# Kernel tuning notes

Hardware: AMD Instinct MI355X
Metric: run time of the kernel (lower is better)

The kernel has to match this reference:

```python
import jax, jax.numpy as jnp
import numpy as np

B, S, E, H, FF = 4, 1024, 1024, 16, 4096
D = E // H
EPS = 1e-5


def layer_norm(x, g, b):
    m = jnp.mean(x, axis=-1, keepdims=True)
    v = jnp.var(x, axis=-1, keepdims=True)
    return (x - m) / jnp.sqrt(v + EPS) * g + b


def setup_inputs() -> dict:
    key = jax.random.key(0)
    ks = jax.random.split(key, 12)
    x = jax.random.normal(ks[0], (B, S, E), dtype=jnp.float32)
    # binary attention mask [B,S,S]; force diagonal=1 so no row is fully masked
    mask = jax.random.randint(ks[1], (B, S, S), 0, 2).astype(jnp.float32)
    idx = jnp.arange(S)
    mask = mask.at[:, idx, idx].set(1.0)
    gnn_adj = jax.random.normal(ks[2], (B, S, S), dtype=jnp.float32) * 0.02
    sc = 0.02
    params = dict(
        Wq=jax.random.normal(ks[3], (E, E), dtype=jnp.float32) * sc, bq=jnp.zeros((E,), jnp.float32),
        Wk=jax.random.normal(ks[4], (E, E), dtype=jnp.float32) * sc, bk=jnp.zeros((E,), jnp.float32),
        Wv=jax.random.normal(ks[5], (E, E), dtype=jnp.float32) * sc, bv=jnp.zeros((E,), jnp.float32),
        Wo=jax.random.normal(ks[6], (E, E), dtype=jnp.float32) * sc, bo=jnp.zeros((E,), jnp.float32),
        g1=jnp.ones((E,), jnp.float32), b1=jnp.zeros((E,), jnp.float32),
        g2=jnp.ones((E,), jnp.float32), b2=jnp.zeros((E,), jnp.float32),
        W1=jax.random.normal(ks[7], (E, FF), dtype=jnp.float32) * sc, bf1=jnp.zeros((FF,), jnp.float32),
        W2=jax.random.normal(ks[8], (FF, E), dtype=jnp.float32) * sc, bf2=jnp.zeros((E,), jnp.float32),
    )
    return dict(x=x, mask=mask, gnn_adj=gnn_adj, **params)


def reference(x, mask, gnn_adj, Wq, bq, Wk, bk, Wv, bv, Wo, bo, g1, b1, g2, b2, W1, bf1, W2, bf2):
    # pre-norm (norm_first=True), dropout = identity (eval)
    nx = layer_norm(x, g1, b1)
    # QKV projections -> [B,H,S,D]
    def split_heads(t):
        return t.reshape(B, S, H, D).transpose(0, 2, 1, 3)
    q = split_heads(nx @ Wq + bq)
    k = split_heads(nx @ Wk + bk)
    v = split_heads(nx @ Wv + bv)
    scores = jnp.einsum('bhqd,bhkd->bhqk', q, k) / jnp.sqrt(jnp.float32(D))
    m = mask[:, None]  # [B,1,S,S]
    scores = jnp.where(m == 0, -jnp.inf, scores * m)
    attn = jax.nn.softmax(scores, axis=-1)
    # non-standard: additive bias AFTER softmax
    attn = attn + gnn_adj[:, None]
    xv = jnp.einsum('bhqk,bhkd->bhqd', attn, v)
    xv = xv.transpose(0, 2, 1, 3).reshape(B, S, E)
    x = x + (xv @ Wo + bo)
    h = layer_norm(x, g2, b2)
    ff = jax.nn.gelu(h @ W1 + bf1, approximate=False) @ W2 + bf2
    return x + ff
```

## Files before the change

kernel.cpp:

```cpp
#include <hip/hip_runtime.h>
#include <hip/hip_bf16.h>

typedef unsigned short u16;
typedef short bf16x8 __attribute__((ext_vector_type(8)));
typedef float f32x4 __attribute__((ext_vector_type(4)));

#define B_ 4
#define S_ 1024
#define E_ 1024
#define H_ 16
#define FF_ 4096
#define D_ 64
#define M_ 4096

__device__ __forceinline__ u16 f2bf(float f) {
  unsigned int u = __builtin_bit_cast(unsigned int, f);
  u += 0x7fffu + ((u >> 16) & 1u);
  return (u16)(u >> 16);
}
__device__ __forceinline__ float bf2f(u16 v) {
  unsigned int u = ((unsigned int)v) << 16;
  return __builtin_bit_cast(float, u);
}

__device__ __forceinline__ void gld_lds16(const void* g, void* l) {
  __builtin_amdgcn_global_load_lds((__attribute__((address_space(1))) void*)g,
                                   (__attribute__((address_space(3))) void*)l,
                                   16, 0, 0);
}

__global__ void __launch_bounds__(256) pre_kernel(
    const float* __restrict__ wq, const float* __restrict__ wk,
    const float* __restrict__ wv, const float* __restrict__ wo,
    const float* __restrict__ w1, const float* __restrict__ w2,
    u16* __restrict__ wt,
    const float* __restrict__ x, const float* __restrict__ g1,
    const float* __restrict__ b1, u16* __restrict__ nx,
    const float* __restrict__ mask, const float* __restrict__ gnn,
    u16* __restrict__ biasI, u16* __restrict__ gnnbf) {
  __shared__ __attribute__((aligned(16))) float smem_f[1088];
  int bid = blockIdx.x;
  int t = threadIdx.x;
  if (bid < 12288) {
    const float* src; u16* dst; int K, N; int local;
    if (bid < 4096) {
      int wsel = bid >> 10; local = bid & 1023; K = 1024; N = 1024;
      src = wsel == 0 ? wq : wsel == 1 ? wk : wsel == 2 ? wv : wo;
      dst = wt + (size_t)wsel * 1024 * 1024;
    } else if (bid < 8192) {
      local = bid - 4096; K = 1024; N = 4096; src = w1;
      dst = wt + (size_t)4 * 1024 * 1024;
    } else {
      local = bid - 8192; K = 4096; N = 1024; src = w2;
      dst = wt + (size_t)8 * 1024 * 1024;
    }
    int tiles_n = N >> 5;
    int n0 = (local % tiles_n) << 5, k0 = (local / tiles_n) << 5;
    float (*tl)[33] = reinterpret_cast<float(*)[33]>(smem_f);
    int tx = t & 31, ty = t >> 5;
#pragma unroll
    for (int i = 0; i < 4; ++i)
      tl[ty + i * 8][tx] = src[(size_t)(k0 + ty + i * 8) * N + n0 + tx];
    __syncthreads();
#pragma unroll
    for (int i = 0; i < 4; ++i)
      dst[(size_t)(n0 + ty + i * 8) * K + k0 + tx] = f2bf(tl[tx][ty + i * 8]);
  } else if (bid < 16384) {
    int row = bid - 12288;
    const float* xr = x + (size_t)row * 1024;
    float4 v = *(const float4*)(xr + t * 4);
    float s = v.x + v.y + v.z + v.w;
    float q = v.x * v.x + v.y * v.y + v.z * v.z + v.w * v.w;
#pragma unroll
    for (int off = 1; off < 64; off <<= 1) {
      s += __shfl_xor(s, off);
      q += __shfl_xor(q, off);
    }
    float* sb = smem_f;
    float* qb = smem_f + 4;
    int w = t >> 6, l = t & 63;
    if (l == 0) { sb[w] = s; qb[w] = q; }
    __syncthreads();
    s = sb[0] + sb[1] + sb[2] + sb[3];
    q = qb[0] + qb[1] + qb[2] + qb[3];
    float mean = s * (1.f / 1024.f);
    float var = q * (1.f / 1024.f) - mean * mean;
    float rs = rsqrtf(var + 1e-5f);
    float4 gv = *(const float4*)(g1 + t * 4);
    float4 bv = *(const float4*)(b1 + t * 4);
    ushort4 o;
    o.x = f2bf((v.x - mean) * rs * gv.x + bv.x);
    o.y = f2bf((v.y - mean) * rs * gv.y + bv.y);
    o.z = f2bf((v.z - mean) * rs * gv.z + bv.z);
    o.w = f2bf((v.w - mean) * rs * gv.w + bv.w);
    *(ushort4*)(nx + (size_t)row * 1024 + t * 4) = o;
  } else {
    int row = bid - 16384;
    int b = row >> 10, q = row & 1023;
    float* mrow = smem_f;
    const float* mp = mask + ((size_t)row << 10);
    const float* gp = gnn + ((size_t)row << 10);
    float4 mv = *(const float4*)(mp + t * 4);
    *(float4*)(mrow + t * 4) = mv;
    float4 gv = *(const float4*)(gp + t * 4);
    ushort4 g4;
    g4.x = f2bf(gv.x); g4.y = f2bf(gv.y); g4.z = f2bf(gv.z); g4.w = f2bf(gv.w);
    *(ushort4*)(gnnbf + ((size_t)row << 10) + t * 4) = g4;
    __syncthreads();
    int kt = t >> 4, c = t & 15;
    const u16 NEG = f2bf(-30008.f);
    const u16 SHIFT = f2bf(-8.0f);
    ushort4 o;
    o.x = (mrow[kt * 64 + c] == 0.f) ? NEG : SHIFT;
    o.y = (mrow[kt * 64 + 16 + c] == 0.f) ? NEG : SHIFT;
    o.z = (mrow[kt * 64 + 32 + c] == 0.f) ? NEG : SHIFT;
    o.w = (mrow[kt * 64 + 48 + c] == 0.f) ? NEG : SHIFT;
    *(ushort4*)(biasI + (((size_t)(b * 16 + kt) << 10) + q) * 64 + c * 4) = o;
  }
}

__global__ void __launch_bounds__(256) vtrans_kernel(
    const u16* __restrict__ v, u16* __restrict__ vt) {
  int st = blockIdx.x, h = blockIdx.y, b = blockIdx.z;
  __shared__ u16 tl[64][72];
  const u16* src = v + ((((size_t)(b * 16 + h)) << 10) + (st << 6)) * 64;
  int r = threadIdx.x >> 2, g = (threadIdx.x & 3) << 4;
  *(uint4*)&tl[r][g] = *(const uint4*)(src + r * 64 + g);
  *(uint4*)&tl[r][g + 8] = *(const uint4*)(src + r * 64 + g + 8);
  __syncthreads();
  u16 tmp[16];
#pragma unroll
  for (int i = 0; i < 16; ++i) tmp[i] = tl[g + i][r];
  u16* dst = vt + ((size_t)b << 20) + (((size_t)(h * 64 + r)) << 10) + (st << 6) + g;
  *(uint4*)(dst) = *(uint4*)(tmp);
  *(uint4*)(dst + 8) = *(uint4*)(tmp + 8);
}

__global__ void __launch_bounds__(256) ln_kernel_b(
    const u16* __restrict__ x, const float* __restrict__ g,
    const float* __restrict__ bt, u16* __restrict__ out) {
  int row = blockIdx.x, t = threadIdx.x;
  const u16* xr = x + ((size_t)row << 10);
  ushort4 xv4 = *(const ushort4*)(xr + t * 4);
  float v0 = bf2f(xv4.x), v1 = bf2f(xv4.y), v2 = bf2f(xv4.z), v3 = bf2f(xv4.w);
  float s = v0 + v1 + v2 + v3;
  float q = v0 * v0 + v1 * v1 + v2 * v2 + v3 * v3;
#pragma unroll
  for (int off = 1; off < 64; off <<= 1) {
    s += __shfl_xor(s, off);
    q += __shfl_xor(q, off);
  }
  __shared__ float sb[4], qb[4];
  int w = t >> 6, l = t & 63;
  if (l == 0) { sb[w] = s; qb[w] = q; }
  __syncthreads();
  s = sb[0] + sb[1] + sb[2] + sb[3];
  q = qb[0] + qb[1] + qb[2] + qb[3];
  float mean = s * (1.f / 1024.f);
  float var = q * (1.f / 1024.f) - mean * mean;
  float rs = rsqrtf(var + 1e-5f);
  float4 gv = *(const float4*)(g + t * 4);
  float4 bv = *(const float4*)(bt + t * 4);
  ushort4 o;
  o.x = f2bf((v0 - mean) * rs * gv.x + bv.x);
  o.y = f2bf((v1 - mean) * rs * gv.y + bv.y);
  o.z = f2bf((v2 - mean) * rs * gv.z + bv.z);
  o.w = f2bf((v3 - mean) * rs * gv.w + bv.w);
  *(ushort4*)(out + ((size_t)row << 10) + t * 4) = o;
}

template <int LDA, int LDB, int NKT>
__device__ __forceinline__ void gemm_core_db64(
    const u16* __restrict__ A, const u16* __restrict__ Bt,
    int bm, int bn, u16* lds, f32x4 acc[4][2]) {
  const int tid = threadIdx.x;
  const int w = tid >> 6, l = tid & 63;
  const int wn = w << 5;
  const int lrow = l >> 3;
  const int cg = (l & 7) ^ lrow;
  const u16* Ab = A + (size_t)(bm << 6) * LDA + (cg << 3);
  const u16* Bb = Bt + (size_t)(bn << 7) * LDB + (cg << 3);
#define GSTAGE64(T, BUF)                                                     \
  {                                                                          \
    const int kk = (T) << 6;                                                 \
    u16* la = lds + (BUF) * 12288;                                           \
    u16* lb = la + 4096;                                                     \
    _Pragma("unroll") for (int i = 0; i < 2; ++i) {                          \
      int c = (w << 1) + i;                                                  \
      int row = (c << 3) + lrow;                                             \
      gld_lds16(Ab + (size_t)row * LDA + kk, la + (c << 9));                 \
    }                                                                        \
    _Pragma("unroll") for (int i = 0; i < 4; ++i) {                          \
      int c = (w << 2) + i;                                                  \
      int row = (c << 3) + lrow;                                             \
      gld_lds16(Bb + (size_t)row * LDB + kk, lb + (c << 9));                 \
    }                                                                        \
  }
  GSTAGE64(0, 0);
  __syncthreads();
  for (int t = 0; t < NKT; ++t) {
    if (t + 1 < NKT) GSTAGE64(t + 1, (t & 1) ^ 1);
    const u16* la = lds + (t & 1) * 12288;
    const u16* lb = la + 4096;
    bf16x8 af[2][4], bfr[2][2];
    const int rr = l & 15;
    const int kgb = l >> 4;
#pragma unroll
    for (int ks = 0; ks < 2; ++ks) {
      const int kg = kgb + (ks << 2);
#pragma unroll
      for (int f = 0; f < 4; ++f) {
        int ra = (f << 4) + rr;
        af[ks][f] = *(const bf16x8*)(la + (ra << 6) + ((kg ^ (ra & 7)) << 3));
      }
#pragma unroll
      for (int f = 0; f < 2; ++f) {
        int rb = wn + (f << 4) + rr;
        bfr[ks][f] = *(const bf16x8*)(lb + (rb << 6) + ((kg ^ (rb & 7)) << 3));
      }
    }
#pragma unroll
    for (int fm = 0; fm < 4; ++fm)
#pragma unroll
      for (int fn = 0; fn < 2; ++fn)
#pragma unroll
        for (int ks = 0; ks < 2; ++ks)
          acc[fm][fn] = __builtin_amdgcn_mfma_f32_16x16x32_bf16(
              af[ks][fm], bfr[ks][fn], acc[fm][fn], 0, 0, 0);
    __syncthreads();
  }
#undef GSTAGE64
}

#define ACC_INIT64()                      \
  f32x4 acc[4][2];                        \
  { f32x4 zf = {0.f, 0.f, 0.f, 0.f};      \
_Pragma("unroll")                         \
    for (int a = 0; a < 4; ++a)           \
_Pragma("unroll")                         \
      for (int bb = 0; bb < 2; ++bb) acc[a][bb] = zf; }

#define EPI_SETUP64()                                   \
  const int w = threadIdx.x >> 6, l = threadIdx.x & 63; \
  const int wn = w << 5;

#define GEMM_LDS64()  __shared__ __attribute__((aligned(16))) u16 lds[2 * 12288]

__global__ void __launch_bounds__(256, 2) gemm_qkv(
    const u16* __restrict__ nx, const u16* __restrict__ wt,
    const float* __restrict__ bq, const float* __restrict__ bk,
    const float* __restrict__ bv, u16* __restrict__ qk, u16* __restrict__ vtmp) {
  GEMM_LDS64();
  ACC_INIT64();
  int z = blockIdx.z;
  const u16* Bt = wt + (size_t)z * 1024 * 1024;
  const float* bias = z == 0 ? bq : z == 1 ? bk : bv;
  u16* out = z == 2 ? vtmp : qk + (size_t)z * M_ * 1024;
  const float scl = (z == 0) ? 0.18033688f : 1.0f;
  gemm_core_db64<1024, 1024, 16>(nx, Bt, blockIdx.x, blockIdx.y, lds, acc);
  EPI_SETUP64();
#pragma unroll
  for (int fm = 0; fm < 4; ++fm)
#pragma unroll
    for (int fn = 0; fn < 2; ++fn)
#pragma unroll
      for (int j = 0; j < 4; ++j) {
        int row = (blockIdx.x << 6) + (fm << 4) + ((l >> 4) << 2) + j;
        int col = (blockIdx.y << 7) + wn + (fn << 4) + (l & 15);
        float v = (acc[fm][fn][j] + bias[col]) * scl;
        int b = row >> 10, s = row & 1023;
        int h = col >> 6, d = col & 63;
        out[(((size_t)(b * 16 + h) << 10) + s) * 64 + d] = f2bf(v);
      }
}

__global__ void __launch_bounds__(256, 2) gemm_gnnv(
    const u16* __restrict__ gnnbf, const u16* __restrict__ vt,
    u16* __restrict__ xvg) {
  GEMM_LDS64();
  ACC_INIT64();
  int b = blockIdx.z;
  const u16* A = gnnbf + ((size_t)b << 20);
  const u16* Bt = vt + ((size_t)b << 20);
  u16* out = xvg + ((size_t)b << 20);
  gemm_core_db64<1024, 1024, 16>(A, Bt, blockIdx.x, blockIdx.y, lds, acc);
  EPI_SETUP64();
#pragma unroll
  for (int fm = 0; fm < 4; ++fm)
#pragma unroll
    for (int fn = 0; fn < 2; ++fn)
#pragma unroll
      for (int j = 0; j < 4; ++j) {
        int row = (blockIdx.x << 6) + (fm << 4) + ((l >> 4) << 2) + j;
        int col = (blockIdx.y << 7) + wn + (fn << 4) + (l & 15);
        out[((size_t)row << 10) + col] = f2bf(acc[fm][fn][j]);
      }
}

__global__ void __launch_bounds__(256, 2) gemm_wo(
    const u16* __restrict__ xv, const u16* __restrict__ wt,
    const float* __restrict__ bo, const float* __restrict__ xres,
    u16* __restrict__ x1b) {
  GEMM_LDS64();
  ACC_INIT64();
  gemm_core_db64<1024, 1024, 16>(xv, wt, blockIdx.x, blockIdx.y, lds, acc);
  EPI_SETUP64();
#pragma unroll
  for (int fm = 0; fm < 4; ++fm)
#pragma unroll
    for (int fn = 0; fn < 2; ++fn)
#pragma unroll
      for (int j = 0; j < 4; ++j) {
        int row = (blockIdx.x << 6) + (fm << 4) + ((l >> 4) << 2) + j;
        int col = (blockIdx.y << 7) + wn + (fn << 4) + (l & 15);
        size_t idx = ((size_t)row << 10) + col;
        x1b[idx] = f2bf(acc[fm][fn][j] + bo[col] + xres[idx]);
      }
}

__global__ void __launch_bounds__(512, 1) gemm_w1_256(
    const u16* __restrict__ hb, const u16* __restrict__ wt,
    const float* __restrict__ bf1, u16* __restrict__ ff1) {
  __shared__ __attribute__((aligned(16))) u16 lds[2 * 16384];
  const int bid = blockIdx.x;
  const int lin = ((bid & 7) << 5) + (bid >> 3);
  const int bm = lin & 15, bn = lin >> 4;
  const int tid = threadIdx.x;
  const int w = tid >> 6, l = tid & 63;
  const int wm = (w >> 2) << 7;
  const int wn = (w & 3) << 6;
  const int lrow3 = l >> 3;
  const int vsw = (l & 7) ^ lrow3;
  const int rpar = vsw >> 2, k8s = vsw & 3;
  const u16* Ab = hb + (size_t)(bm << 8) * 1024 + k8s * 8;
  const u16* Bb = wt + (size_t)(bn << 8) * 1024 + k8s * 8;

  f32x4 acc[8][4];
  {
    f32x4 zf = {0.f, 0.f, 0.f, 0.f};
#pragma unroll
    for (int a = 0; a < 8; ++a)
#pragma unroll
      for (int bb2 = 0; bb2 < 4; ++bb2) acc[a][bb2] = zf;
  }

#define GSTAGE256(T, BUF)                                                    \
  {                                                                          \
    const int kk = (T) << 5;                                                 \
    u16* la = lds + (BUF) * 16384;                                           \
    u16* lb = la + 8192;                                                     \
    _Pragma("unroll") for (int i = 0; i < 2; ++i) {                          \
      int c = (w << 1) + i;                                       \
      int row = ((c << 3) + lrow3) * 2 + rpar;                               \
      gld_lds16(Ab + (size_t)row * 1024 + kk, la + (c << 9) + (l << 3));     \
      gld_lds16(Bb + (size_t)row * 1024 + kk, lb + (c << 9) + (l << 3));     \
    }                                                                        \
  }

  GSTAGE256(0, 0);
  __syncthreads();

  const int rr = l & 15;
  const int kg = l >> 4;
  for (int t = 0; t < 32; ++t) {
    if (t + 1 < 32) GSTAGE256(t + 1, (t & 1) ^ 1);
    const u16* la = lds + (t & 1) * 16384;
    const u16* lb = la + 8192;
    bf16x8 bfr[4];
#pragma unroll
    for (int fn = 0; fn < 4; ++fn) {
      int rb = wn + (fn << 4) + rr;
      int slot = (((rb & 1) << 2) | kg) ^ ((rb >> 1) & 7);
      bfr[fn] = *(const bf16x8*)(lb + ((rb >> 1) << 6) + (slot << 3));
    }
#pragma unroll
    for (int fm = 0; fm < 8; ++fm) {
      int ra = wm + (fm << 4) + rr;
      int slot = (((ra & 1) << 2) | kg) ^ ((ra >> 1) & 7);
      bf16x8 afr = *(const bf16x8*)(la + ((ra >> 1) << 6) + (slot << 3));
#pragma unroll
      for (int fn = 0; fn < 4; ++fn)
        acc[fm][fn] = __builtin_amdgcn_mfma_f32_16x16x32_bf16(
            afr, bfr[fn], acc[fm][fn], 0, 0, 0);
    }
    __syncthreads();
  }
#undef GSTAGE256
#pragma unroll
  for (int fm = 0; fm < 8; ++fm)
#pragma unroll
    for (int fn = 0; fn < 4; ++fn)
#pragma unroll
      for (int j = 0; j < 4; ++j) {
        int row = (bm << 8) + wm + (fm << 4) + ((l >> 4) << 2) + j;
        int col = (bn << 8) + wn + (fn << 4) + (l & 15);
        float v = acc[fm][fn][j] + bf1[col];
        float ge = 0.5f * v * (1.f + erff(v * 0.70710678118654752f));
        ff1[((size_t)row << 12) + col] = f2bf(ge);
      }
}

__global__ void __launch_bounds__(256, 2) gemm_w2(
    const u16* __restrict__ ff1, const u16* __restrict__ wt,
    const float* __restrict__ bf2, const u16* __restrict__ x1b,
    float* __restrict__ out) {
  GEMM_LDS64();
  ACC_INIT64();
  gemm_core_db64<4096, 4096, 64>(ff1, wt, blockIdx.x, blockIdx.y, lds, acc);
  EPI_SETUP64();
#pragma unroll
  for (int fm = 0; fm < 4; ++fm)
#pragma unroll
    for (int fn = 0; fn < 2; ++fn)
#pragma unroll
      for (int j = 0; j < 4; ++j) {
        int row = (blockIdx.x << 6) + (fm << 4) + ((l >> 4) << 2) + j;
        int col = (blockIdx.y << 7) + wn + (fn << 4) + (l & 15);
        size_t idx = ((size_t)row << 10) + col;
        out[idx] = acc[fm][fn][j] + bf2[col] + bf2f(x1b[idx]);
      }
}

__global__ void __launch_bounds__(256, 2) attn_kernel(
    const u16* __restrict__ Q, const u16* __restrict__ K,
    const u16* __restrict__ Vt, const u16* __restrict__ biasI,
    const u16* __restrict__ xvg, u16* __restrict__ xv) {
  const int lin = ((blockIdx.x & 7) << 6) + (blockIdx.x >> 3);
  const int qt = lin & 7, h = (lin >> 3) & 15, b = lin >> 7;
  const int tid = threadIdx.x, w = tid >> 6, l = tid & 63;
  __shared__ __attribute__((aligned(16))) u16 kbuf[2][64 * 64];
  __shared__ __attribute__((aligned(16))) u16 vbuf[2][64 * 64];
  __shared__ __attribute__((aligned(16))) u16 pbuf[4][32 * 64];
  const size_t bh = ((size_t)(b * 16 + h)) << 16;
  const u16* Qb = Q + bh;
  const u16* Kb = K + bh;
  const u16* Vtb = Vt + ((size_t)b << 20) + ((size_t)(h * 64) << 10);
  const u16* biasb = biasI + ((size_t)b << 20);
  const int q0 = (qt << 7) + (w << 5);
  const int lrow = l >> 3, cg = (l & 7) ^ lrow;
  const int l4 = l >> 4, lo = l & 15;
  u16* p_w = pbuf[w];

  bf16x8 qf[2][2];
#pragma unroll
  for (int m = 0; m < 2; ++m)
#pragma unroll
    for (int ks = 0; ks < 2; ++ks)
      qf[m][ks] = *(const bf16x8*)(Qb + ((size_t)(q0 + m * 16 + lo) << 6) +
                                   l4 * 8 + ks * 32);
  bf16x8 onesf;
#pragma unroll
  for (int j = 0; j < 8; ++j) onesf[j] = (short)0x3F80;

  f32x4 osoft[2][4], osum[2];
  f32x4 zf = {0.f, 0.f, 0.f, 0.f};
#pragma unroll
  for (int m = 0; m < 2; ++m) {
    osum[m] = zf;
#pragma unroll
    for (int fd = 0; fd < 4; ++fd) osoft[m][fd] = zf;
  }

#define STAGE(T, BUF)                                                          \
  {                                                                            \
    int kv0s = (T) << 6;                                                       \
    u16* kd = &kbuf[BUF][0];                                                   \
    u16* vd = &vbuf[BUF][0];                                                   \
    _Pragma("unroll") for (int i = 0; i < 2; ++i) {                            \
      int c = (w << 1) + i;                                                    \
      gld_lds16(Kb + ((size_t)(kv0s + (c << 3) + lrow) << 6) + (cg << 3),      \
                kd + (c << 9));                                                \
      gld_lds16(Vtb + ((size_t)((c << 3) + lrow) << 10) + kv0s + (cg << 3),    \
                vd + (c << 9));                                                \
    }                                                                          \
  }

  STAGE(0, 0);
  __syncthreads();

  for (int t = 0; t < 16; ++t) {
    const int cur = t & 1;
    if (t < 15) STAGE(t + 1, cur ^ 1);
    const u16* kb_ = &kbuf[cur][0];
    const u16* vb_ = &vbuf[cur][0];
    f32x4 sacc[2][4];
#pragma unroll
    for (int m = 0; m < 2; ++m)
#pragma unroll
      for (int j = 0; j < 4; ++j) {
        ushort4 bb = *(const ushort4*)(
            biasb + (((size_t)(t * 1024 + q0 + m * 16 + l4 * 4 + j)) << 6) +
            lo * 4);
        sacc[m][0][j] = bf2f(bb.x);
        sacc[m][1][j] = bf2f(bb.y);
        sacc[m][2][j] = bf2f(bb.z);
        sacc[m][3][j] = bf2f(bb.w);
      }
    __builtin_amdgcn_s_setprio(1);
#pragma unroll
    for (int ks = 0; ks < 2; ++ks) {
      const int kg = l4 + (ks << 2);
      bf16x8 kf[4];
#pragma unroll
      for (int fn = 0; fn < 4; ++fn) {
        int rk = (fn << 4) + lo;
        kf[fn] = *(const bf16x8*)(kb_ + (rk << 6) + ((kg ^ (rk & 7)) << 3));
      }
#pragma unroll
      for (int m = 0; m < 2; ++m)
#pragma unroll
        for (int fn = 0; fn < 4; ++fn)
          sacc[m][fn] = __builtin_amdgcn_mfma_f32_16x16x32_bf16(
              qf[m][ks], kf[fn], sacc[m][fn], 0, 0, 0);
    }
    __builtin_amdgcn_s_setprio(0);
#pragma unroll
    for (int m = 0; m < 2; ++m)
#pragma unroll
      for (int fn = 0; fn < 4; ++fn)
#pragma unroll
        for (int j = 0; j < 4; ++j) {
          float p = exp2f(sacc[m][fn][j]);
          unsigned int u = __builtin_bit_cast(unsigned int, p);
          int prow = (m << 4) + (l4 << 2) + j;
          int pcol = (fn << 4) + lo;
          p_w[(prow << 6) + (pcol ^ ((prow & 7) << 3))] =
              (u16)((u + 0x8000u) >> 16);
        }
    __builtin_amdgcn_s_setprio(1);
#pragma unroll
    for (int ks = 0; ks < 2; ++ks) {
      const int kg = l4 + (ks << 2);
      bf16x8 pf[2], vf[4];
#pragma unroll
      for (int m = 0; m < 2; ++m) {
        int pr = (m << 4) + lo;
        pf[m] = *(const bf16x8*)(p_w + (pr << 6) + ((kg ^ (pr & 7)) << 3));
      }
#pragma unroll
      for (int fd = 0; fd < 4; ++fd) {
        int rd = (fd << 4) + lo;
        vf[fd] = *(const bf16x8*)(vb_ + (rd << 6) + ((kg ^ (rd & 7)) << 3));
      }
#pragma unroll
      for (int m = 0; m < 2; ++m) {
        osum[m] = __builtin_amdgcn_mfma_f32_16x16x32_bf16(
            pf[m], onesf, osum[m], 0, 0, 0);
#pragma unroll
        for (int fd = 0; fd < 4; ++fd)
          osoft[m][fd] = __builtin_amdgcn_mfma_f32_16x16x32_bf16(
              pf[m], vf[fd], osoft[m][fd], 0, 0, 0);
      }
    }
    __builtin_amdgcn_s_setprio(0);
    __syncthreads();
  }
#pragma unroll
  for (int m = 0; m < 2; ++m) {
    f32x4 rl;
#pragma unroll
    for (int j = 0; j < 4; ++j) rl[j] = 1.0f / osum[m][j];
#pragma unroll
    for (int fd = 0; fd < 4; ++fd)
#pragma unroll
      for (int j = 0; j < 4; ++j) {
        int qrow = q0 + (m << 4) + (l4 << 2) + j;
        int e = (h << 6) + (fd << 4) + lo;
        size_t idx = (((size_t)(b * 1024 + qrow)) << 10) + e;
        float o = osoft[m][fd][j] * rl[j] + bf2f(xvg[idx]);
        xv[idx] = f2bf(o);
      }
  }
#undef STAGE
}

extern "C" void kernel_launch(void* const* d_in, const int* in_sizes, int n_in,
                              void* d_out, int out_size, void* d_ws, size_t ws_size,
                              hipStream_t stream) {
  (void)in_sizes; (void)n_in; (void)out_size; (void)ws_size;
  const float* x   = (const float*)d_in[0];
  const float* mask= (const float*)d_in[1];
  const float* gnn = (const float*)d_in[2];
  const float* Wq  = (const float*)d_in[3];
  const float* bq  = (const float*)d_in[4];
  const float* Wk  = (const float*)d_in[5];
  const float* bk  = (const float*)d_in[6];
  const float* Wv  = (const float*)d_in[7];
  const float* bv  = (const float*)d_in[8];
  const float* Wo  = (const float*)d_in[9];
  const float* bo  = (const float*)d_in[10];
  const float* g1  = (const float*)d_in[11];
  const float* b1  = (const float*)d_in[12];
  const float* g2  = (const float*)d_in[13];
  const float* b2  = (const float*)d_in[14];
  const float* W1  = (const float*)d_in[15];
  const float* bf1 = (const float*)d_in[16];
  const float* W2  = (const float*)d_in[17];
  const float* bf2 = (const float*)d_in[18];
  float* out = (float*)d_out;

  char* ws = (char*)d_ws;
  const size_t MB = 1024 * 1024;
  u16*  wt    = (u16*)(ws);
  u16*  nx    = (u16*)(ws + 24 * MB);
  u16*  xvbuf = (u16*)(ws + 24 * MB);
  u16*  hbuf  = (u16*)(ws + 24 * MB);
  u16*  qk    = (u16*)(ws + 32 * MB);
  u16*  vt    = (u16*)(ws + 48 * MB);
  u16*  biasI = (u16*)(ws + 56 * MB);
  u16*  gnnbf = (u16*)(ws + 64 * MB);
  u16*  x1b   = (u16*)(ws + 64 * MB);
  u16*  vtmp  = (u16*)(ws + 72 * MB);
  u16*  xvg   = (u16*)(ws + 72 * MB);
  u16*  ff1   = (u16*)(ws + 32 * MB);

  pre_kernel<<<20480, 256, 0, stream>>>(Wq, Wk, Wv, Wo, W1, W2, wt,
                                        x, g1, b1, nx, mask, gnn, biasI, gnnbf);
  gemm_qkv<<<dim3(64, 8, 3), 256, 0, stream>>>(nx, wt, bq, bk, bv, qk, vtmp);
  vtrans_kernel<<<dim3(16, 16, 4), 256, 0, stream>>>(vtmp, vt);
  gemm_gnnv<<<dim3(16, 8, 4), 256, 0, stream>>>(gnnbf, vt, xvg);
  attn_kernel<<<512, 256, 0, stream>>>(
      qk, qk + (size_t)4 * MB, vt, biasI, xvg, xvbuf);
  gemm_wo<<<dim3(64, 8), 256, 0, stream>>>(xvbuf, wt + (size_t)3 * MB, bo, x, x1b);
  ln_kernel_b<<<4096, 256, 0, stream>>>(x1b, g2, b2, hbuf);
  gemm_w1_256<<<256, 512, 0, stream>>>(hbuf, wt + (size_t)4 * MB, bf1, ff1);
  gemm_w2<<<dim3(64, 8), 256, 0, stream>>>(ff1, wt + (size_t)8 * MB, bf2, x1b, out);
}
```

Baseline: 231.9 us.

## Triple-buffer FFN GEMM pipelines with explicit waitcnt and barrier control

Both FFN GEMMs (W1 and W2) switch from double-buffered LDS staging to a three-stage ring. Prefetches run two K-tiles ahead, and fine-grained s_waitcnt vmcnt plus raw s_barrier replace __syncthreads. MFMA sections are raised in priority with s_setprio. The aim is to hide global-load latency better, at the cost of more dynamic LDS per block, which may limit occupancy.

New measurement: 229.9 us. About the same (-0.9%).

```diff
diff --git a/kernel.cpp b/kernel.cpp
--- a/kernel.cpp
+++ b/kernel.cpp
@@ -232,6 +232,85 @@
 #undef GSTAGE64
 }
 
+template <int LDA, int LDB, int NKT>
+__device__ __forceinline__ void gemm_core_p3(
+    const u16* __restrict__ A, const u16* __restrict__ Bt,
+    int bm, int bn, u16* lds, f32x4 acc[4][2]) {
+  const int tid = threadIdx.x;
+  const int w = tid >> 6, l = tid & 63;
+  const int wn = w << 5;
+  const int lrow = l >> 3;
+  const int cg = (l & 7) ^ lrow;
+  const u16* Ab = A + (size_t)(bm << 6) * LDA + (cg << 3);
+  const u16* Bb = Bt + (size_t)(bn << 7) * LDB + (cg << 3);
+#define PSTAGE(T, BUF)                                                       \
+  {                                                                          \
+    const int kk = (T) << 6;                                                 \
+    u16* la = lds + (BUF) * 12288;                                           \
+    u16* lb = la + 4096;                                                     \
+    _Pragma("unroll") for (int i = 0; i < 2; ++i) {                          \
+      int c = (w << 1) + i;                                                  \
+      int row = (c << 3) + lrow;                                             \
+      gld_lds16(Ab + (size_t)row * LDA + kk, la + (c << 9));                 \
+    }                                                                        \
+    _Pragma("unroll") for (int i = 0; i < 4; ++i) {                          \
+      int c = (w << 2) + i;                                                  \
+      int row = (c << 3) + lrow;                                             \
+      gld_lds16(Bb + (size_t)row * LDB + kk, lb + (c << 9));                 \
+    }                                                                        \
+  }
+  PSTAGE(0, 0);
+  PSTAGE(1, 1);
+  int cur = 0;
+  for (int t = 0; t < NKT; ++t) {
+    if (t + 2 < NKT) {
+      int nb = cur + 2; if (nb >= 3) nb -= 3;
+      PSTAGE(t + 2, nb);
+      asm volatile("s_waitcnt vmcnt(12)" ::: "memory");
+    } else if (t + 1 < NKT) {
+      asm volatile("s_waitcnt vmcnt(6)" ::: "memory");
+    } else {
+      asm volatile("s_waitcnt vmcnt(0)" ::: "memory");
+    }
+    __builtin_amdgcn_sched_barrier(0);
+    __builtin_amdgcn_s_barrier();
+    const u16* la = lds + cur * 12288;
+    const u16* lb = la + 4096;
+    bf16x8 af[2][4], bfr[2][2];
+    const int rr = l & 15;
+    const int kgb = l >> 4;
+#pragma unroll
+    for (int ks = 0; ks < 2; ++ks) {
+      const int kg = kgb + (ks << 2);
+#pragma unroll
+      for (int f = 0; f < 4; ++f) {
+        int ra = (f << 4) + rr;
+        af[ks][f] = *(const bf16x8*)(la + (ra << 6) + ((kg ^ (ra & 7)) << 3));
+      }
+#pragma unroll
+      for (int f = 0; f < 2; ++f) {
+        int rb = wn + (f << 4) + rr;
+        bfr[ks][f] = *(const bf16x8*)(lb + (rb << 6) + ((kg ^ (rb & 7)) << 3));
+      }
+    }
+    __builtin_amdgcn_s_setprio(1);
+#pragma unroll
+    for (int fm = 0; fm < 4; ++fm)
+#pragma unroll
+      for (int fn = 0; fn < 2; ++fn)
+#pragma unroll
+        for (int ks = 0; ks < 2; ++ks)
+          acc[fm][fn] = __builtin_amdgcn_mfma_f32_16x16x32_bf16(
+              af[ks][fm], bfr[ks][fn], acc[fm][fn], 0, 0, 0);
+    __builtin_amdgcn_s_setprio(0);
+    asm volatile("s_waitcnt lgkmcnt(0)" ::: "memory");
+    __builtin_amdgcn_sched_barrier(0);
+    __builtin_amdgcn_s_barrier();
+    cur = (cur == 2) ? 0 : cur + 1;
+  }
+#undef PSTAGE
+}
+
 #define ACC_INIT64()                      \
   f32x4 acc[4][2];                        \
   { f32x4 zf = {0.f, 0.f, 0.f, 0.f};      \
@@ -318,10 +397,10 @@
       }
 }
 
-__global__ void __launch_bounds__(512, 1) gemm_w1_256(
+__global__ void __launch_bounds__(512, 1) gemm_w1_256p(
     const u16* __restrict__ hb, const u16* __restrict__ wt,
     const float* __restrict__ bf1, u16* __restrict__ ff1) {
-  __shared__ __attribute__((aligned(16))) u16 lds[2 * 16384];
+  extern __shared__ __attribute__((aligned(16))) u16 lds[];
   const int bid = blockIdx.x;
   const int lin = ((bid & 7) << 5) + (bid >> 3);
   const int bm = lin & 15, bn = lin >> 4;
@@ -344,27 +423,37 @@
       for (int bb2 = 0; bb2 < 4; ++bb2) acc[a][bb2] = zf;
   }
 
-#define GSTAGE256(T, BUF)                                                    \
+#define WSTAGE(T, BUF)                                                       \
   {                                                                          \
     const int kk = (T) << 5;                                                 \
     u16* la = lds + (BUF) * 16384;                                           \
     u16* lb = la + 8192;                                                     \
     _Pragma("unroll") for (int i = 0; i < 2; ++i) {                          \
-      int c = (w << 1) + i;                                       \
+      int c = (w << 1) + i;                                                  \
       int row = ((c << 3) + lrow3) * 2 + rpar;                               \
       gld_lds16(Ab + (size_t)row * 1024 + kk, la + (c << 9) + (l << 3));     \
       gld_lds16(Bb + (size_t)row * 1024 + kk, lb + (c << 9) + (l << 3));     \
     }                                                                        \
   }
 
-  GSTAGE256(0, 0);
-  __syncthreads();
-
+  WSTAGE(0, 0);
+  WSTAGE(1, 1);
+  int cur = 0;
   const int rr = l & 15;
   const int kg = l >> 4;
   for (int t = 0; t < 32; ++t) {
-    if (t + 1 < 32) GSTAGE256(t + 1, (t & 1) ^ 1);
-    const u16* la = lds + (t & 1) * 16384;
+    if (t + 2 < 32) {
+      int nb = cur + 2; if (nb >= 3) nb -= 3;
+      WSTAGE(t + 2, nb);
+      asm volatile("s_waitcnt vmcnt(8)" ::: "memory");
+    } else if (t + 1 < 32) {
+      asm volatile("s_waitcnt vmcnt(4)" ::: "memory");
+    } else {
+      asm volatile("s_waitcnt vmcnt(0)" ::: "memory");
+    }
+    __builtin_amdgcn_sched_barrier(0);
+    __builtin_amdgcn_s_barrier();
+    const u16* la = lds + cur * 16384;
     const u16* lb = la + 8192;
     bf16x8 bfr[4];
 #pragma unroll
@@ -373,6 +462,7 @@
       int slot = (((rb & 1) << 2) | kg) ^ ((rb >> 1) & 7);
       bfr[fn] = *(const bf16x8*)(lb + ((rb >> 1) << 6) + (slot << 3));
     }
+    __builtin_amdgcn_s_setprio(1);
 #pragma unroll
     for (int fm = 0; fm < 8; ++fm) {
       int ra = wm + (fm << 4) + rr;
@@ -383,9 +473,13 @@
         acc[fm][fn] = __builtin_amdgcn_mfma_f32_16x16x32_bf16(
             afr, bfr[fn], acc[fm][fn], 0, 0, 0);
     }
-    __syncthreads();
-  }
-#undef GSTAGE256
+    __builtin_amdgcn_s_setprio(0);
+    asm volatile("s_waitcnt lgkmcnt(0)" ::: "memory");
+    __builtin_amdgcn_sched_barrier(0);
+    __builtin_amdgcn_s_barrier();
+    cur = (cur == 2) ? 0 : cur + 1;
+  }
+#undef WSTAGE
 #pragma unroll
   for (int fm = 0; fm < 8; ++fm)
 #pragma unroll
@@ -404,9 +498,9 @@
     const u16* __restrict__ ff1, const u16* __restrict__ wt,
     const float* __restrict__ bf2, const u16* __restrict__ x1b,
     float* __restrict__ out) {
-  GEMM_LDS64();
+  extern __shared__ __attribute__((aligned(16))) u16 lds[];
   ACC_INIT64();
-  gemm_core_db64<4096, 4096, 64>(ff1, wt, blockIdx.x, blockIdx.y, lds, acc);
+  gemm_core_p3<4096, 4096, 64>(ff1, wt, blockIdx.x, blockIdx.y, lds, acc);
   EPI_SETUP64();
 #pragma unroll
   for (int fm = 0; fm < 4; ++fm)
@@ -623,6 +717,6 @@
       qk, qk + (size_t)4 * MB, vt, biasI, xvg, xvbuf);
   gemm_wo<<<dim3(64, 8), 256, 0, stream>>>(xvbuf, wt + (size_t)3 * MB, bo, x, x1b);
   ln_kernel_b<<<4096, 256, 0, stream>>>(x1b, g2, b2, hbuf);
-  gemm_w1_256<<<256, 512, 0, stream>>>(hbuf, wt + (size_t)4 * MB, bf1, ff1);
-  gemm_w2<<<dim3(64, 8), 256, 0, stream>>>(ff1, wt + (size_t)8 * MB, bf2, x1b, out);
-}
+  gemm_w1_256p<<<256, 512, 3 * 32768, stream>>>(hbuf, wt + (size_t)4 * MB, bf1, ff1);
+  gemm_w2<<<dim3(64, 8), 256, 3 * 24576, stream>>>(ff1, wt + (size_t)8 * MB, bf2, x1b, out);
+}
```
